# Optimization experiments

Measured on AMD Instinct MI355X. Metric: run time of the kernel, lower is better.

## Reference

```python
import jax, jax.numpy as jnp
import numpy as np

B, C, OUT, H, W, M1, M2, HID = 4, 64, 64, 256, 256, 32, 32, 64
COORD = C + 1  # MLP input: channels + 1 coordinate


def _lin(key, fan_in, fan_out):
    lim = 1.0 / np.sqrt(fan_in)
    kw, kb = jax.random.split(key)
    Wm = jax.random.uniform(kw, (fan_in, fan_out), minval=-lim, maxval=lim, dtype=jnp.float32)
    b = jax.random.uniform(kb, (fan_out,), minval=-lim, maxval=lim, dtype=jnp.float32)
    return Wm, b


def setup_inputs() -> dict:
    key = jax.random.key(0)
    ks = jax.random.split(key, 12)
    x = jax.random.normal(ks[0], (B, C, H, W), dtype=jnp.float32)
    # basis_w MLP: (C+1) -> HID -> HID -> 2*M2
    wW0, wb0 = _lin(ks[1], COORD, HID)
    wW1, wb1 = _lin(ks[2], HID, HID)
    wW2, wb2 = _lin(ks[3], HID, 2 * M2)
    # basis_h MLP: (C+1) -> HID -> HID -> 2*M1
    hW0, hb0 = _lin(ks[4], COORD, HID)
    hW1, hb1 = _lin(ks[5], HID, HID)
    hW2, hb2 = _lin(ks[6], HID, 2 * M1)
    std = (1.0 / (C + OUT)) ** 0.5
    Wf_re = std * jax.random.normal(ks[7], (C, OUT, M1, M2), dtype=jnp.float32)
    Wf_im = std * jax.random.normal(ks[8], (C, OUT, M1, M2), dtype=jnp.float32)
    mixer_w, mixer_b = _lin(ks[9], OUT, OUT)
    mixer_w = mixer_w.T  # (out, in) conv1x1 layout
    sc_w, sc_b = _lin(ks[10], C, OUT)
    sc_w = sc_w.T
    return {
        "x": x,
        "wW0": wW0, "wb0": wb0, "wW1": wW1, "wb1": wb1, "wW2": wW2, "wb2": wb2,
        "hW0": hW0, "hb0": hb0, "hW1": hW1, "hb1": hb1, "hW2": hW2, "hb2": hb2,
        "Wf_re": Wf_re, "Wf_im": Wf_im,
        "mixer_w": mixer_w, "mixer_b": mixer_b,
        "sc_w": sc_w, "sc_b": sc_b,
    }


def _gelu(v):
    return jax.nn.gelu(v, approximate=False)  # torch GELU is exact erf


def _cmlp(x, W0, b0, W1, b1, W2, b2, m):
    h = _gelu(x @ W0 + b0)
    h = _gelu(h @ W1 + b1)
    o = h @ W2 + b2
    return jax.lax.complex(o[..., :m], o[..., m:])


def reference(x, wW0, wb0, wW1, wb1, wW2, wb2,
              hW0, hb0, hW1, hb1, hW2, hb2,
              Wf_re, Wf_im, mixer_w, mixer_b, sc_w, sc_b):
    Bb, Cc, Hh, Ww = x.shape
    # --- W-direction basis: input is (values, w-coord) per pixel ---
    wc = jnp.linspace(-1.0, 1.0, Ww, dtype=jnp.float32)
    w_in = jnp.concatenate(
        [jnp.transpose(x, (0, 2, 3, 1)),
         jnp.broadcast_to(wc[None, None, :, None], (Bb, Hh, Ww, 1))], axis=-1)
    wb = _cmlp(w_in, wW0, wb0, wW1, wb1, wW2, wb2, M2)  # (B,H,W,m2) complex
    xc = x.astype(jnp.complex64)
    # separable transform along W: contract W against runtime basis
    tfw = jnp.einsum('bchw,bhwm->bchm', xc, wb)  # (B,C,H,m2)
    # --- H-direction basis: input is real part of W-transform + h-coord ---
    hcv = jnp.linspace(-1.0, 1.0, Hh, dtype=jnp.float32)
    h_in = jnp.concatenate(
        [jnp.transpose(tfw.real, (0, 3, 2, 1)),
         jnp.broadcast_to(hcv[None, None, :, None], (Bb, M2, Hh, 1))], axis=-1)
    hb = _cmlp(h_in, hW0, hb0, hW1, hb1, hW2, hb2, M1)  # (B,m2,H,m1) complex
    tfhw = jnp.einsum('bchm,bmhk->bckm', tfw, hb)  # (B,C,m1,m2)
    Wf = jax.lax.complex(Wf_re, Wf_im)  # (C_in, C_out, m1, m2)
    proc = jnp.einsum('bixy,oixy->boxy', tfhw, Wf)  # (B,out,m1,m2)
    # inverse transforms with conjugate-transposed bases
    rec = jnp.einsum('bokm,bmhk->bohm', proc, jnp.conj(hb))  # (B,out,H,m2)
    spatial = jnp.einsum('bohm,bhwm->bohw', rec, jnp.conj(wb)).real / (Hh * Ww)
    y = jnp.einsum('bchw,oc->bohw', spatial, mixer_w) + mixer_b[None, :, None, None]
    y = _gelu(y)
    y = y + jnp.einsum('bchw,oc->bohw', x, sc_w) + sc_b[None, :, None, None]
    return _gelu(y)
```

## Files before the change

### kernel.cpp

```cpp
#include <hip/hip_runtime.h>
#include <math.h>


typedef __attribute__((ext_vector_type(8))) short bf16x8;
typedef __attribute__((ext_vector_type(4))) float f32x4;

__device__ __forceinline__ float gelu_f(float v) {
    const float u = v * 0.70710678118654752440f;
    const float xa = fabsf(u);
    const float t = __builtin_amdgcn_rcpf(fmaf(0.3275911f, xa, 1.0f));
    float p = fmaf(1.061405429f, t, -1.453152027f);
    p = fmaf(p, t, 1.421413741f);
    p = fmaf(p, t, -0.284496736f);
    p = fmaf(p, t, 0.254829592f);
    p *= t;
    const float e = __expf(-xa * xa);
    float erfv = fmaf(-p, e, 1.0f);
    erfv = (u < 0.0f) ? -erfv : erfv;
    return 0.5f * v * (1.0f + erfv);
}

__device__ __forceinline__ unsigned short f2b(float f) {
    union { float f; unsigned int u; } v; v.f = f;
    unsigned int u = v.u + 0x7FFFu + ((v.u >> 16) & 1u);
    return (unsigned short)(u >> 16);
}
__device__ __forceinline__ float b2f(unsigned short b) {
    union { unsigned int u; float f; } v; v.u = ((unsigned int)b) << 16;
    return v.f;
}

__device__ __forceinline__ void stage_xT(const float* __restrict__ x,
    unsigned short* __restrict__ sA, int b, int h, int w0, int t, int LD)
{
    const int lane = t & 63, wv = t >> 6;
    const int g = lane >> 4, wg = lane & 15;
#pragma unroll
    for (int r = 0; r < 4; ++r) {
        const int cb = r * 16 + wv * 4;
        const float4 v = *(const float4*)&x[((size_t)(b * 64 + cb + g) * 256 + h) * 256 + w0 + wg * 4];
        const float bx = __shfl_xor(v.x, 16);
        const float by = __shfl_xor(v.y, 16);
        const float bz = __shfl_xor(v.z, 16);
        const float bw = __shfl_xor(v.w, 16);
        float4 s1;
        s1.x = ((g & 1) == 0) ? v.x : by;
        s1.y = ((g & 1) == 0) ? bx  : v.y;
        s1.z = ((g & 1) == 0) ? v.z : bw;
        s1.w = ((g & 1) == 0) ? bz  : v.w;
        const float cx = __shfl_xor(s1.x, 32);
        const float cy = __shfl_xor(s1.y, 32);
        const float cz = __shfl_xor(s1.z, 32);
        const float cw = __shfl_xor(s1.w, 32);
        float4 s2;
        s2.x = ((g & 2) == 0) ? s1.x : cz;
        s2.y = ((g & 2) == 0) ? s1.y : cw;
        s2.z = ((g & 2) == 0) ? cx   : s1.z;
        s2.w = ((g & 2) == 0) ? cy   : s1.w;
        ushort4 u;
        u.x = f2b(s2.x); u.y = f2b(s2.y); u.z = f2b(s2.z); u.w = f2b(s2.w);
        *(ushort4*)&sA[(wg * 4 + g) * LD + cb] = u;
    }
}

__global__ void k_prep(const float* __restrict__ wW0, const float* __restrict__ wW1,
                       const float* __restrict__ wW2,
                       const float* __restrict__ hW0, const float* __restrict__ hW1,
                       const float* __restrict__ hW2,
                       unsigned short* __restrict__ wT0, unsigned short* __restrict__ wT1,
                       unsigned short* __restrict__ wT2,
                       unsigned short* __restrict__ hT0, unsigned short* __restrict__ hT1,
                       unsigned short* __restrict__ hT2)
{
    const int t = threadIdx.x;
    for (int idx = t; idx < 64 * 96; idx += 256) {
        const int o = idx / 96, k = idx % 96;
        wT0[idx] = (k < 65) ? f2b(wW0[k * 64 + o]) : (unsigned short)0;
        hT0[idx] = (k < 65) ? f2b(hW0[k * 64 + o]) : (unsigned short)0;
    }
    for (int idx = t; idx < 4096; idx += 256) {
        const int o = idx >> 6, k = idx & 63;
        wT1[idx] = f2b(wW1[k * 64 + o]);
        wT2[idx] = f2b(wW2[k * 64 + o]);
        hT1[idx] = f2b(hW1[k * 64 + o]);
        hT2[idx] = f2b(hW2[k * 64 + o]);
    }
}

__global__ __launch_bounds__(256) void k_psum(const float* __restrict__ src,
                                              float* __restrict__ dst,
                                              int nparts, int part_stride)
{
    const int i = (blockIdx.x * 256 + threadIdx.x) * 4;
    float4 acc = *(const float4*)&src[i];
    for (int p = 1; p < nparts; ++p) {
        const float4 v = *(const float4*)&src[(size_t)p * part_stride + i];
        acc.x += v.x; acc.y += v.y; acc.z += v.z; acc.w += v.w;
    }
    *(float4*)&dst[i] = acc;
}

__global__ __launch_bounds__(256) void k_psum_procT(const float* __restrict__ src,
                                                    float* __restrict__ dst)
{
    const int idx = blockIdx.x * 256 + threadIdx.x;
    const int o = idx & 63, k = (idx >> 6) & 31, m = (idx >> 11) & 31, b = idx >> 16;
    const size_t in = (size_t)(b * 64 + o) * 1024 + k * 32 + m;
    const float re = src[in] + src[524288 + in];
    const float im = src[262144 + in] + src[524288 + 262144 + in];
    dst[idx] = re;
    dst[262144 + idx] = im;
}

constexpr int MLD = 104;

template<bool GELU, int NKC>
__device__ __forceinline__ void mfma_layer(
    const unsigned short* __restrict__ sW,
    const unsigned short* __restrict__ sAct,
    unsigned short* __restrict__ dst,
    const float* __restrict__ bias, int lane, int wv)
{
    const int arow = lane & 15;
    const int koff = (lane >> 4) * 8;
    const int crow = 16 * wv + (lane >> 4) * 4;
    const f32x4 zero = {0.f, 0.f, 0.f, 0.f};
    f32x4 acc[4] = {zero, zero, zero, zero};
#pragma unroll
    for (int kc = 0; kc < NKC; ++kc) {
        const bf16x8 a = *(const bf16x8*)&sW[(16 * wv + arow) * MLD + kc * 32 + koff];
#pragma unroll
        for (int nt = 0; nt < 4; ++nt) {
            const bf16x8 b = *(const bf16x8*)&sAct[(nt * 16 + arow) * MLD + kc * 32 + koff];
            acc[nt] = __builtin_amdgcn_mfma_f32_16x16x32_bf16(a, b, acc[nt], 0, 0, 0);
        }
    }
    const float4 bv = *(const float4*)&bias[crow];
#pragma unroll
    for (int nt = 0; nt < 4; ++nt) {
        const int px = nt * 16 + arow;
        float v0 = acc[nt][0] + bv.x;
        float v1 = acc[nt][1] + bv.y;
        float v2 = acc[nt][2] + bv.z;
        float v3 = acc[nt][3] + bv.w;
        if (GELU) { v0 = gelu_f(v0); v1 = gelu_f(v1); v2 = gelu_f(v2); v3 = gelu_f(v3); }
        ushort4 u;
        u.x = f2b(v0); u.y = f2b(v1); u.z = f2b(v2); u.w = f2b(v3);
        *(ushort4*)&dst[px * MLD + crow] = u;
    }
}

__device__ __forceinline__ void stage_wT96(const unsigned short* __restrict__ src,
                                           unsigned short* __restrict__ sW, int t) {
#pragma unroll
    for (int r = 0; r < 3; ++r) {
        const int idx = r * 256 + t;
        const int row = idx / 12, f = idx % 12;
        *(uint4*)&sW[row * MLD + f * 8] = *(const uint4*)&src[row * 96 + f * 8];
    }
}
__device__ __forceinline__ void stage_wT64(const unsigned short* __restrict__ src,
                                           unsigned short* __restrict__ sW, int t) {
#pragma unroll
    for (int r = 0; r < 2; ++r) {
        const int idx = r * 256 + t;
        const int row = idx >> 3, f = idx & 7;
        *(uint4*)&sW[row * MLD + f * 8] = *(const uint4*)&src[row * 64 + f * 8];
    }
}

__global__ __launch_bounds__(256) void k_wb_mlp2(
    const float* __restrict__ x,
    const unsigned short* __restrict__ wT0, const float* __restrict__ b0,
    const unsigned short* __restrict__ wT1, const float* __restrict__ b1,
    const unsigned short* __restrict__ wT2, const float* __restrict__ b2,
    unsigned short* __restrict__ wb_bf, unsigned short* __restrict__ wbT)
{
    __shared__ __align__(16) unsigned short sA[64 * MLD];
    __shared__ __align__(16) unsigned short sB[64 * MLD];
    __shared__ __align__(16) unsigned short sW[64 * MLD];
    const int blk = blockIdx.x;
    const int b = blk >> 10, h = (blk >> 2) & 255, wq = blk & 3;
    const int w0 = wq * 64;
    const int t = threadIdx.x;
    const int lane = t & 63, wv = t >> 6;

    stage_xT(x, sA, b, h, w0, t, MLD);
    if (t < 64) {
        const uint4 z = {0, 0, 0, 0};
        *(uint4*)&sA[t * MLD + 64] = z;
        *(uint4*)&sA[t * MLD + 72] = z;
        *(uint4*)&sA[t * MLD + 80] = z;
        *(uint4*)&sA[t * MLD + 88] = z;
        sA[t * MLD + 64] = f2b((float)(w0 + t) * (2.0f / 255.0f) - 1.0f);
    }
    stage_wT96(wT0, sW, t);
    __syncthreads();
    mfma_layer<true, 3>(sW, sA, sB, b0, lane, wv);
    __syncthreads();
    stage_wT64(wT1, sW, t);
    __syncthreads();
    mfma_layer<true, 2>(sW, sB, sA, b1, lane, wv);
    __syncthreads();
    stage_wT64(wT2, sW, t);
    __syncthreads();
    {
        const int arow = lane & 15;
        const int koff = (lane >> 4) * 8;
        const int crow = 16 * wv + (lane >> 4) * 4;
        const f32x4 zero = {0.f, 0.f, 0.f, 0.f};
        f32x4 acc[4] = {zero, zero, zero, zero};
#pragma unroll
        for (int kc = 0; kc < 2; ++kc) {
            const bf16x8 a = *(const bf16x8*)&sW[(16 * wv + arow) * MLD + kc * 32 + koff];
#pragma unroll
            for (int nt = 0; nt < 4; ++nt) {
                const bf16x8 bb = *(const bf16x8*)&sA[(nt * 16 + arow) * MLD + kc * 32 + koff];
                acc[nt] = __builtin_amdgcn_mfma_f32_16x16x32_bf16(a, bb, acc[nt], 0, 0, 0);
            }
        }
        const float4 bv = *(const float4*)&b2[crow];
        const size_t tb2 = (size_t)(b * 256 + h) * 16384;
#pragma unroll
        for (int nt = 0; nt < 4; ++nt) {
            const int px = nt * 16 + arow;
            ushort4 u;
            u.x = f2b(acc[nt][0] + bv.x);
            u.y = f2b(acc[nt][1] + bv.y);
            u.z = f2b(acc[nt][2] + bv.z);
            u.w = f2b(acc[nt][3] + bv.w);
            *(ushort4*)&sB[px * MLD + crow] = u;
            wbT[tb2 + (size_t)(crow + 0) * 256 + w0 + px] = u.x;
            wbT[tb2 + (size_t)(crow + 1) * 256 + w0 + px] = u.y;
            wbT[tb2 + (size_t)(crow + 2) * 256 + w0 + px] = u.z;
            wbT[tb2 + (size_t)(crow + 3) * 256 + w0 + px] = u.w;
        }
    }
    __syncthreads();

    const size_t pixbase = (size_t)(b * 256 + h) * 256 + w0;
#pragma unroll
    for (int r = 0; r < 2; ++r) {
        const int idx = r * 256 + t;
        const int px = idx >> 3, f = idx & 7;
        *(uint4*)&wb_bf[(pixbase + px) * 64 + f * 8] = *(const uint4*)&sB[px * MLD + f * 8];
    }
}

__global__ __launch_bounds__(256) void k_tfw2(
    const float* __restrict__ x,
    const unsigned short* __restrict__ wbT,
    float* __restrict__ tfwM)
{
    constexpr int TLD = 264;
    __shared__ __align__(16) unsigned short sW[64 * TLD];
    __shared__ __align__(16) unsigned short sX[64 * TLD];
    const int bh = blockIdx.x;
    const int b = bh >> 8, h = bh & 255;
    const int t = threadIdx.x;
    const int lane = t & 63, wv = t >> 6;

    const size_t wtb = (size_t)bh * 16384;
#pragma unroll
    for (int r = 0; r < 8; ++r) {
        const int idx = r * 256 + t;
        const int row = idx >> 5, f = idx & 31;
        *(uint4*)&sW[row * TLD + f * 8] = *(const uint4*)&wbT[wtb + (size_t)row * 256 + f * 8];
    }
#pragma unroll
    for (int r = 0; r < 16; ++r) {
        const int idx = r * 256 + t;
        const int c = idx >> 6, f = idx & 63;
        const float4 v = *(const float4*)&x[((size_t)(b * 64 + c) * 256 + h) * 256 + f * 4];
        ushort4 u; u.x = f2b(v.x); u.y = f2b(v.y); u.z = f2b(v.z); u.w = f2b(v.w);
        *(ushort4*)&sX[c * TLD + f * 4] = u;
    }
    __syncthreads();

    const int arow = lane & 15;
    const int koff = (lane >> 4) * 8;
    const f32x4 zero = {0.f, 0.f, 0.f, 0.f};
    f32x4 acc[4] = {zero, zero, zero, zero};
#pragma unroll
    for (int kc = 0; kc < 8; ++kc) {
        const bf16x8 a = *(const bf16x8*)&sW[(16 * wv + arow) * TLD + kc * 32 + koff];
#pragma unroll
        for (int nt = 0; nt < 4; ++nt) {
            const bf16x8 bb = *(const bf16x8*)&sX[(nt * 16 + arow) * TLD + kc * 32 + koff];
            acc[nt] = __builtin_amdgcn_mfma_f32_16x16x32_bf16(a, bb, acc[nt], 0, 0, 0);
        }
    }
    __syncthreads();
    float* sF = (float*)sW;
    const int crow = 16 * wv + (lane >> 4) * 4;
#pragma unroll
    for (int nt = 0; nt < 4; ++nt) {
        const int c = nt * 16 + arow;
#pragma unroll
        for (int j = 0; j < 4; ++j)
            sF[(crow + j) * 68 + c] = acc[nt][j];
    }
    __syncthreads();
#pragma unroll
    for (int r = 0; r < 4; ++r) {
        const int idx = r * 256 + t;
        const int m = idx >> 5, g = idx & 31;
        float4 v;
        v.x = sF[m * 68 + g * 2];
        v.y = sF[(m + 32) * 68 + g * 2];
        v.z = sF[m * 68 + g * 2 + 1];
        v.w = sF[(m + 32) * 68 + g * 2 + 1];
        *(float4*)&tfwM[((size_t)(b * 32 + m) * 256 + h) * 128 + g * 4] = v;
    }
}

__global__ __launch_bounds__(256) void k_hb_mlp2(
    const float* __restrict__ tfwM,
    const unsigned short* __restrict__ hT0, const float* __restrict__ b0,
    const unsigned short* __restrict__ hT1, const float* __restrict__ b1,
    const unsigned short* __restrict__ hT2, const float* __restrict__ b2,
    unsigned short* __restrict__ hb_bf)
{
    __shared__ __align__(16) unsigned short sA[64 * MLD];
    __shared__ __align__(16) unsigned short sB[64 * MLD];
    __shared__ __align__(16) unsigned short sW[64 * MLD];
    const int blk = blockIdx.x;
    const int bm = blk >> 2, hq = blk & 3;
    const int h0 = hq * 64;
    const int t = threadIdx.x;
    const int lane = t & 63, wv = t >> 6;

#pragma unroll
    for (int r = 0; r < 4; ++r) {
        const int idx = r * 256 + t;
        const int p = idx >> 4, f = idx & 15;
        const float* src = &tfwM[(size_t)(bm * 256 + h0 + p) * 128 + f * 8];
        const float4 u0 = *(const float4*)&src[0];
        const float4 u1 = *(const float4*)&src[4];
        ushort4 u;
        u.x = f2b(u0.x); u.y = f2b(u0.z); u.z = f2b(u1.x); u.w = f2b(u1.z);
        *(ushort4*)&sA[p * MLD + f * 4] = u;
    }
    if (t < 64) {
        const uint4 z = {0, 0, 0, 0};
        *(uint4*)&sA[t * MLD + 64] = z;
        *(uint4*)&sA[t * MLD + 72] = z;
        *(uint4*)&sA[t * MLD + 80] = z;
        *(uint4*)&sA[t * MLD + 88] = z;
        sA[t * MLD + 64] = f2b((float)(h0 + t) * (2.0f / 255.0f) - 1.0f);
    }
    stage_wT96(hT0, sW, t);
    __syncthreads();
    mfma_layer<true, 3>(sW, sA, sB, b0, lane, wv);
    __syncthreads();
    stage_wT64(hT1, sW, t);
    __syncthreads();
    mfma_layer<true, 2>(sW, sB, sA, b1, lane, wv);
    __syncthreads();
    stage_wT64(hT2, sW, t);
    __syncthreads();
    mfma_layer<false, 2>(sW, sA, sB, b2, lane, wv);
    __syncthreads();

    const size_t pixbase = (size_t)bm * 256 + h0;
#pragma unroll
    for (int r = 0; r < 2; ++r) {
        const int idx = r * 256 + t;
        const int px = idx >> 3, f = idx & 7;
        *(uint4*)&hb_bf[(pixbase + px) * 64 + f * 8] = *(const uint4*)&sB[px * MLD + f * 8];
    }
}

__global__ __launch_bounds__(256) void k_tfhw3(
    const float* __restrict__ tfwM,
    const unsigned short* __restrict__ hb_bf,
    float* __restrict__ tfhw_p)
{
    __shared__ float hr[64 * 32];
    __shared__ float hi2[64 * 32];
    __shared__ float slab[32 * 64];
    const int blk = blockIdx.x;
    const int bm = blk >> 3, chalf = (blk >> 2) & 1, hq = blk & 3;
    const int b = bm >> 5, m = bm & 31;
    const int t = threadIdx.x;
#pragma unroll
    for (int r = 0; r < 2; ++r) {
        const int q = r * 256 + t;
        const int hl = q >> 3, f = q & 7;
        const uint4 raw = *(const uint4*)&hb_bf[((size_t)bm * 256 + hq * 64 + hl) * 64 + f * 8];
        const unsigned short* us = (const unsigned short*)&raw;
        float v[8];
#pragma unroll
        for (int j = 0; j < 8; ++j) v[j] = b2f(us[j]);
        float* dst = (f < 4) ? &hr[hl * 32 + f * 8] : &hi2[hl * 32 + (f - 4) * 8];
        float4 lo; lo.x = v[0]; lo.y = v[1]; lo.z = v[2]; lo.w = v[3];
        float4 hi; hi.x = v[4]; hi.y = v[5]; hi.z = v[6]; hi.w = v[7];
        *(float4*)&dst[0] = lo;
        *(float4*)&dst[4] = hi;
    }
    const int k = t & 31, cq = t >> 5;
    float accr[4] = {0.f, 0.f, 0.f, 0.f}, acci[4] = {0.f, 0.f, 0.f, 0.f};
    const size_t tbase = (size_t)bm * 32768;
    for (int ht = 0; ht < 2; ++ht) {
        __syncthreads();
#pragma unroll
        for (int r = 0; r < 2; ++r) {
            const int q = r * 256 + t;
            const int hl = q >> 3, f = q & 7;
            *(float4*)&slab[hl * 64 + f * 4] =
                *(const float4*)&tfwM[tbase + (size_t)(hq * 64 + ht * 32 + hl) * 128 + chalf * 64 + f * 4];
        }
        __syncthreads();
#pragma unroll 8
        for (int hl = 0; hl < 32; ++hl) {
            const float hrv = hr[(ht * 32 + hl) * 32 + k];
            const float hiv = hi2[(ht * 32 + hl) * 32 + k];
            const float4 u0 = *(const float4*)&slab[hl * 64 + cq * 8];
            const float4 u1 = *(const float4*)&slab[hl * 64 + cq * 8 + 4];
            accr[0] = fmaf(u0.x, hrv, fmaf(-u0.y, hiv, accr[0]));
            acci[0] = fmaf(u0.x, hiv, fmaf( u0.y, hrv, acci[0]));
            accr[1] = fmaf(u0.z, hrv, fmaf(-u0.w, hiv, accr[1]));
            acci[1] = fmaf(u0.z, hiv, fmaf( u0.w, hrv, acci[1]));
            accr[2] = fmaf(u1.x, hrv, fmaf(-u1.y, hiv, accr[2]));
            acci[2] = fmaf(u1.x, hiv, fmaf( u1.y, hrv, acci[2]));
            accr[3] = fmaf(u1.z, hrv, fmaf(-u1.w, hiv, accr[3]));
            acci[3] = fmaf(u1.z, hiv, fmaf( u1.w, hrv, acci[3]));
        }
    }
    float* tp = tfhw_p + (size_t)hq * 524288;
#pragma unroll
    for (int i = 0; i < 4; ++i) {
        const int c = chalf * 32 + cq * 4 + i;
        const size_t po = ((size_t)(b * 64 + c) * 32 + k) * 32 + m;
        tp[po] = accr[i];
        tp[262144 + po] = acci[i];
    }
}

__global__ __launch_bounds__(256) void k_proc2(
    const float* __restrict__ tfhw,
    const float* __restrict__ Wf_re, const float* __restrict__ Wf_im,
    float* __restrict__ proc_p)
{
    const int blk = blockIdx.x;
    const int o = blk >> 3, kq = (blk >> 1) & 3, chalf = blk & 1;
    const int t = threadIdx.x;
    const int mo = kq * 256 + t;
    const float* tre = tfhw;
    const float* tim = tfhw + 262144;
    float accr[4] = {0.f, 0.f, 0.f, 0.f}, acci[4] = {0.f, 0.f, 0.f, 0.f};
    for (int cc = 0; cc < 32; ++cc) {
        const int c = chalf * 32 + cc;
        const float wfr = Wf_re[(size_t)(c * 64 + o) * 1024 + mo];
        const float wfi = Wf_im[(size_t)(c * 64 + o) * 1024 + mo];
#pragma unroll
        for (int bb = 0; bb < 4; ++bb) {
            const float tr = tre[(size_t)(bb * 64 + c) * 1024 + mo];
            const float ti = tim[(size_t)(bb * 64 + c) * 1024 + mo];
            accr[bb] = fmaf(tr, wfr, fmaf(-ti, wfi, accr[bb]));
            acci[bb] = fmaf(tr, wfi, fmaf(ti, wfr, acci[bb]));
        }
    }
    float* pp = proc_p + (size_t)chalf * 524288;
#pragma unroll
    for (int bb = 0; bb < 4; ++bb) {
        pp[(size_t)(bb * 64 + o) * 1024 + mo] = accr[bb];
        pp[262144 + (size_t)(bb * 64 + o) * 1024 + mo] = acci[bb];
    }
}

__global__ __launch_bounds__(256) void k_rec4(
    const float* __restrict__ procT,
    const unsigned short* __restrict__ hb_bf,
    unsigned short* __restrict__ recO)
{
    __shared__ float lhr[32 * 32];
    __shared__ float lhi[32 * 32];
    const int blk = blockIdx.x;
    const int bm = blk >> 3, hq = blk & 7;
    const int b = bm >> 5, m = bm & 31;
    const int t = threadIdx.x;
    {
        const int hl = t >> 3, f = t & 7;
        const uint4 raw = *(const uint4*)&hb_bf[((size_t)bm * 256 + hq * 32 + hl) * 64 + f * 8];
        const unsigned short* us = (const unsigned short*)&raw;
        float v[8];
#pragma unroll
        for (int j = 0; j < 8; ++j) v[j] = b2f(us[j]);
        float* dst = (f < 4) ? &lhr[hl * 32 + f * 8] : &lhi[hl * 32 + (f - 4) * 8];
        float4 lo; lo.x = v[0]; lo.y = v[1]; lo.z = v[2]; lo.w = v[3];
        float4 hi; hi.x = v[4]; hi.y = v[5]; hi.z = v[6]; hi.w = v[7];
        *(float4*)&dst[0] = lo;
        *(float4*)&dst[4] = hi;
    }
    const int o = t & 63, hg = t >> 6;
    const float* pr = procT + (size_t)(b * 32 + m) * 2048 + o;
    const float* pi = pr + 262144;
    float Pr[32], Pi[32];
#pragma unroll
    for (int k = 0; k < 32; ++k) {
        Pr[k] = pr[k * 64];
        Pi[k] = pi[k * 64];
    }
    __syncthreads();
    for (int hh = 0; hh < 8; ++hh) {
        const int hl = hg * 8 + hh;
        float ar = 0.f, ai = 0.f;
#pragma unroll
        for (int k4 = 0; k4 < 8; ++k4) {
            const float4 hr4 = *(const float4*)&lhr[hl * 32 + k4 * 4];
            const float4 hi4 = *(const float4*)&lhi[hl * 32 + k4 * 4];
            ar = fmaf(Pr[k4*4+0], hr4.x, fmaf(Pi[k4*4+0], hi4.x, ar));
            ai = fmaf(Pi[k4*4+0], hr4.x, fmaf(-Pr[k4*4+0], hi4.x, ai));
            ar = fmaf(Pr[k4*4+1], hr4.y, fmaf(Pi[k4*4+1], hi4.y, ar));
            ai = fmaf(Pi[k4*4+1], hr4.y, fmaf(-Pr[k4*4+1], hi4.y, ai));
            ar = fmaf(Pr[k4*4+2], hr4.z, fmaf(Pi[k4*4+2], hi4.z, ar));
            ai = fmaf(Pi[k4*4+2], hr4.z, fmaf(-Pr[k4*4+2], hi4.z, ai));
            ar = fmaf(Pr[k4*4+3], hr4.w, fmaf(Pi[k4*4+3], hi4.w, ar));
            ai = fmaf(Pi[k4*4+3], hr4.w, fmaf(-Pr[k4*4+3], hi4.w, ai));
        }
        const int h = hq * 32 + hl;
        const size_t rb = ((size_t)(b * 256 + h) * 64 + o) * 64;
        recO[rb + m]      = f2b(ar);
        recO[rb + 32 + m] = f2b(ai);
    }
}

__global__ __launch_bounds__(256) void k_final4(
    const float* __restrict__ x,
    const unsigned short* __restrict__ wb_bf,
    const unsigned short* __restrict__ recO,
    const float* __restrict__ mw, const float* __restrict__ mb,
    const float* __restrict__ scw, const float* __restrict__ scb,
    float* __restrict__ out)
{
    constexpr int LD = 72;
    __shared__ __align__(16) unsigned short sWb[64 * LD];
    __shared__ __align__(16) unsigned short sR [64 * LD];
    __shared__ __align__(16) unsigned short sX [64 * LD];
    __shared__ __align__(16) unsigned short sS [64 * LD];
    const int blk = blockIdx.x;
    const int b = blk >> 10, h = (blk >> 2) & 255, wq = blk & 3;
    const int w0 = wq * 64;
    const int t = threadIdx.x;
    const int lane = t & 63, wv = t >> 6;
    const size_t pixbase = (size_t)(b * 256 + h) * 256 + w0;

#pragma unroll
    for (int r = 0; r < 2; ++r) {
        const int idx = r * 256 + t;
        const int px = idx >> 3, f = idx & 7;
        *(uint4*)&sWb[px * LD + f * 8] = *(const uint4*)&wb_bf[(pixbase + px) * 64 + f * 8];
    }
    const size_t recbase = (size_t)(b * 256 + h) * 4096;
#pragma unroll
    for (int r = 0; r < 2; ++r) {
        const int idx = r * 256 + t;
        const int o = idx >> 3, f = idx & 7;
        *(uint4*)&sR[o * LD + f * 8] = *(const uint4*)&recO[recbase + (size_t)o * 64 + f * 8];
    }
    stage_xT(x, sX, b, h, w0, t, LD);
    __syncthreads();

    const int arow = lane & 15;
    const int koff = (lane >> 4) * 8;
    const f32x4 zero = {0.f, 0.f, 0.f, 0.f};

    f32x4 accA[4] = {zero, zero, zero, zero};
#pragma unroll
    for (int kc = 0; kc < 2; ++kc) {
        const bf16x8 a = *(const bf16x8*)&sR[(16 * wv + arow) * LD + kc * 32 + koff];
#pragma unroll
        for (int nt = 0; nt < 4; ++nt) {
            const bf16x8 bb = *(const bf16x8*)&sWb[(nt * 16 + arow) * LD + kc * 32 + koff];
            accA[nt] = __builtin_amdgcn_mfma_f32_16x16x32_bf16(a, bb, accA[nt], 0, 0, 0);
        }
    }
    __syncthreads();

    const int crow = 16 * wv + (lane >> 4) * 4;
#pragma unroll
    for (int nt = 0; nt < 4; ++nt) {
        const int px = nt * 16 + arow;
#pragma unroll
        for (int j = 0; j < 4; ++j)
            sS[px * LD + crow + j] = f2b(accA[nt][j] * (1.0f / 65536.0f));
    }
#pragma unroll
    for (int r = 0; r < 4; ++r) {
        const int idx = r * 256 + t;
        const int o = idx >> 4, cq = idx & 15;
        const float4 v1 = *(const float4*)&mw[o * 64 + cq * 4];
        ushort4 u1;
        u1.x = f2b(v1.x); u1.y = f2b(v1.y); u1.z = f2b(v1.z); u1.w = f2b(v1.w);
        *(ushort4*)&sWb[o * LD + cq * 4] = u1;
        const float4 v2 = *(const float4*)&scw[o * 64 + cq * 4];
        ushort4 u2;
        u2.x = f2b(v2.x); u2.y = f2b(v2.y); u2.z = f2b(v2.z); u2.w = f2b(v2.w);
        *(ushort4*)&sR[o * LD + cq * 4] = u2;
    }
    __syncthreads();

    f32x4 accB[4] = {zero, zero, zero, zero};
    f32x4 accC[4] = {zero, zero, zero, zero};
#pragma unroll
    for (int kc = 0; kc < 2; ++kc) {
        const bf16x8 am = *(const bf16x8*)&sWb[(16 * wv + arow) * LD + kc * 32 + koff];
        const bf16x8 as = *(const bf16x8*)&sR [(16 * wv + arow) * LD + kc * 32 + koff];
#pragma unroll
        for (int nt = 0; nt < 4; ++nt) {
            const bf16x8 bs = *(const bf16x8*)&sS[(nt * 16 + arow) * LD + kc * 32 + koff];
            const bf16x8 bx = *(const bf16x8*)&sX[(nt * 16 + arow) * LD + kc * 32 + koff];
            accB[nt] = __builtin_amdgcn_mfma_f32_16x16x32_bf16(am, bs, accB[nt], 0, 0, 0);
            accC[nt] = __builtin_amdgcn_mfma_f32_16x16x32_bf16(as, bx, accC[nt], 0, 0, 0);
        }
    }

#pragma unroll
    for (int nt = 0; nt < 4; ++nt) {
        const int px = nt * 16 + arow;
#pragma unroll
        for (int j = 0; j < 4; ++j) {
            const int o = crow + j;
            const float y = gelu_f(accB[nt][j] + mb[o]);
            const float z = y + accC[nt][j] + scb[o];
            out[((size_t)(b * 64 + o) * 256 + h) * 256 + w0 + px] = gelu_f(z);
        }
    }
}

extern "C" void kernel_launch(void* const* d_in, const int* in_sizes, int n_in,
                              void* d_out, int out_size, void* d_ws, size_t ws_size,
                              hipStream_t stream) {
    const float* x    = (const float*)d_in[0];
    const float* wW0  = (const float*)d_in[1];
    const float* wb0  = (const float*)d_in[2];
    const float* wW1  = (const float*)d_in[3];
    const float* wb1  = (const float*)d_in[4];
    const float* wW2  = (const float*)d_in[5];
    const float* wb2  = (const float*)d_in[6];
    const float* hW0  = (const float*)d_in[7];
    const float* hb0  = (const float*)d_in[8];
    const float* hW1  = (const float*)d_in[9];
    const float* hb1  = (const float*)d_in[10];
    const float* hW2  = (const float*)d_in[11];
    const float* hb2  = (const float*)d_in[12];
    const float* Wf_re = (const float*)d_in[13];
    const float* Wf_im = (const float*)d_in[14];
    const float* mw   = (const float*)d_in[15];
    const float* mbv  = (const float*)d_in[16];
    const float* scw  = (const float*)d_in[17];
    const float* scb  = (const float*)d_in[18];

    char* base = (char*)d_ws;
    unsigned short* wb_bf = (unsigned short*)(base + 0);
    unsigned short* wbT   = (unsigned short*)(base + 33554432);
    float* tfwM   = (float*)(base + 67108864);
    unsigned short* hb_bf = (unsigned short*)(base + 83886080);
    float* tfhw_p = (float*)(base + 88080384);
    float* tfhw   = (float*)(base + 96468992);
    float* proc_p = (float*)(base + 98566144);
    float* procT  = (float*)(base + 102760448);
    unsigned short* recO = (unsigned short*)(base + 104857600);
    unsigned short* wT0 = (unsigned short*)(base + 113246208);
    unsigned short* wT1 = (unsigned short*)(base + 113258496);
    unsigned short* wT2 = (unsigned short*)(base + 113266688);
    unsigned short* hT0 = (unsigned short*)(base + 113274880);
    unsigned short* hT1 = (unsigned short*)(base + 113287168);
    unsigned short* hT2 = (unsigned short*)(base + 113295360);

    k_prep<<<1, 256, 0, stream>>>(wW0, wW1, wW2, hW0, hW1, hW2,
                                  wT0, wT1, wT2, hT0, hT1, hT2);
    k_wb_mlp2<<<4096, 256, 0, stream>>>(x, wT0, wb0, wT1, wb1, wT2, wb2, wb_bf, wbT);
    k_tfw2<<<1024, 256, 0, stream>>>(x, wbT, tfwM);
    k_hb_mlp2<<<512, 256, 0, stream>>>(tfwM, hT0, hb0, hT1, hb1, hT2, hb2, hb_bf);
    k_tfhw3<<<1024, 256, 0, stream>>>(tfwM, hb_bf, tfhw_p);
    k_psum<<<1024, 256, 0, stream>>>(tfhw_p, tfhw, 4, 524288);
    k_proc2<<<512, 256, 0, stream>>>(tfhw, Wf_re, Wf_im, proc_p);
    k_psum_procT<<<1024, 256, 0, stream>>>(proc_p, procT);
    k_rec4<<<1024, 256, 0, stream>>>(procT, hb_bf, recO);
    k_final4<<<4096, 256, 0, stream>>>(x, wb_bf, recO, mw, mbv, scw, scb, (float*)d_out);
}
```

Baseline: 195.5 us.

## Fuse W-basis MLP with W-direction transform to drop transposed basis buffer

```diff
diff --git a/kernel.cpp b/kernel.cpp
--- a/kernel.cpp
+++ b/kernel.cpp
@@ -30,36 +30,44 @@
     return v.f;
 }
 
+constexpr int MLD = 104;
+constexpr int XLD = 72;
+
+__device__ __forceinline__ ushort4 butterfly_xT(const float4 v, int q) {
+    const float bx = __shfl_xor(v.x, 1);
+    const float by = __shfl_xor(v.y, 1);
+    const float bz = __shfl_xor(v.z, 1);
+    const float bw = __shfl_xor(v.w, 1);
+    float4 s1;
+    s1.x = ((q & 1) == 0) ? v.x : by;
+    s1.y = ((q & 1) == 0) ? bx  : v.y;
+    s1.z = ((q & 1) == 0) ? v.z : bw;
+    s1.w = ((q & 1) == 0) ? bz  : v.w;
+    const float cx = __shfl_xor(s1.x, 2);
+    const float cy = __shfl_xor(s1.y, 2);
+    const float cz = __shfl_xor(s1.z, 2);
+    const float cw = __shfl_xor(s1.w, 2);
+    float4 s2;
+    s2.x = ((q & 2) == 0) ? s1.x : cz;
+    s2.y = ((q & 2) == 0) ? s1.y : cw;
+    s2.z = ((q & 2) == 0) ? cx   : s1.z;
+    s2.w = ((q & 2) == 0) ? cy   : s1.w;
+    ushort4 u;
+    u.x = f2b(s2.x); u.y = f2b(s2.y); u.z = f2b(s2.z); u.w = f2b(s2.w);
+    return u;
+}
+
 __device__ __forceinline__ void stage_xT(const float* __restrict__ x,
     unsigned short* __restrict__ sA, int b, int h, int w0, int t, int LD)
 {
     const int lane = t & 63, wv = t >> 6;
-    const int g = lane >> 4, wg = lane & 15;
+    const int q = lane & 3, wg = lane >> 2;
 #pragma unroll
     for (int r = 0; r < 4; ++r) {
-        const int cb = r * 16 + wv * 4;
-        const float4 v = *(const float4*)&x[((size_t)(b * 64 + cb + g) * 256 + h) * 256 + w0 + wg * 4];
-        const float bx = __shfl_xor(v.x, 16);
-        const float by = __shfl_xor(v.y, 16);
-        const float bz = __shfl_xor(v.z, 16);
-        const float bw = __shfl_xor(v.w, 16);
-        float4 s1;
-        s1.x = ((g & 1) == 0) ? v.x : by;
-        s1.y = ((g & 1) == 0) ? bx  : v.y;
-        s1.z = ((g & 1) == 0) ? v.z : bw;
-        s1.w = ((g & 1) == 0) ? bz  : v.w;
-        const float cx = __shfl_xor(s1.x, 32);
-        const float cy = __shfl_xor(s1.y, 32);
-        const float cz = __shfl_xor(s1.z, 32);
-        const float cw = __shfl_xor(s1.w, 32);
-        float4 s2;
-        s2.x = ((g & 2) == 0) ? s1.x : cz;
-        s2.y = ((g & 2) == 0) ? s1.y : cw;
-        s2.z = ((g & 2) == 0) ? cx   : s1.z;
-        s2.w = ((g & 2) == 0) ? cy   : s1.w;
-        ushort4 u;
-        u.x = f2b(s2.x); u.y = f2b(s2.y); u.z = f2b(s2.z); u.w = f2b(s2.w);
-        *(ushort4*)&sA[(wg * 4 + g) * LD + cb] = u;
+        const int cb = (r * 4 + wv) * 4;
+        const float4 v = *(const float4*)&x[((size_t)(b * 64 + cb + q) * 256 + h) * 256 + w0 + wg * 4];
+        const ushort4 u = butterfly_xT(v, q);
+        *(ushort4*)&sA[(wg * 4 + q) * LD + cb] = u;
     }
 }
 
@@ -111,8 +119,6 @@
     dst[idx] = re;
     dst[262144 + idx] = im;
 }
-
-constexpr int MLD = 104;
 
 template<bool GELU, int NKC>
 __device__ __forceinline__ void mfma_layer(
@@ -169,136 +175,120 @@
     }
 }
 
-__global__ __launch_bounds__(256) void k_wb_mlp2(
+__global__ __launch_bounds__(256) void k_wbtfw(
     const float* __restrict__ x,
     const unsigned short* __restrict__ wT0, const float* __restrict__ b0,
     const unsigned short* __restrict__ wT1, const float* __restrict__ b1,
     const unsigned short* __restrict__ wT2, const float* __restrict__ b2,
-    unsigned short* __restrict__ wb_bf, unsigned short* __restrict__ wbT)
-{
-    __shared__ __align__(16) unsigned short sA[64 * MLD];
-    __shared__ __align__(16) unsigned short sB[64 * MLD];
-    __shared__ __align__(16) unsigned short sW[64 * MLD];
-    const int blk = blockIdx.x;
-    const int b = blk >> 10, h = (blk >> 2) & 255, wq = blk & 3;
-    const int w0 = wq * 64;
-    const int t = threadIdx.x;
-    const int lane = t & 63, wv = t >> 6;
-
-    stage_xT(x, sA, b, h, w0, t, MLD);
-    if (t < 64) {
-        const uint4 z = {0, 0, 0, 0};
-        *(uint4*)&sA[t * MLD + 64] = z;
-        *(uint4*)&sA[t * MLD + 72] = z;
-        *(uint4*)&sA[t * MLD + 80] = z;
-        *(uint4*)&sA[t * MLD + 88] = z;
-        sA[t * MLD + 64] = f2b((float)(w0 + t) * (2.0f / 255.0f) - 1.0f);
-    }
-    stage_wT96(wT0, sW, t);
-    __syncthreads();
-    mfma_layer<true, 3>(sW, sA, sB, b0, lane, wv);
-    __syncthreads();
-    stage_wT64(wT1, sW, t);
-    __syncthreads();
-    mfma_layer<true, 2>(sW, sB, sA, b1, lane, wv);
-    __syncthreads();
-    stage_wT64(wT2, sW, t);
-    __syncthreads();
-    {
-        const int arow = lane & 15;
-        const int koff = (lane >> 4) * 8;
-        const int crow = 16 * wv + (lane >> 4) * 4;
-        const f32x4 zero = {0.f, 0.f, 0.f, 0.f};
-        f32x4 acc[4] = {zero, zero, zero, zero};
-#pragma unroll
-        for (int kc = 0; kc < 2; ++kc) {
-            const bf16x8 a = *(const bf16x8*)&sW[(16 * wv + arow) * MLD + kc * 32 + koff];
-#pragma unroll
-            for (int nt = 0; nt < 4; ++nt) {
-                const bf16x8 bb = *(const bf16x8*)&sA[(nt * 16 + arow) * MLD + kc * 32 + koff];
-                acc[nt] = __builtin_amdgcn_mfma_f32_16x16x32_bf16(a, bb, acc[nt], 0, 0, 0);
-            }
-        }
-        const float4 bv = *(const float4*)&b2[crow];
-        const size_t tb2 = (size_t)(b * 256 + h) * 16384;
-#pragma unroll
-        for (int nt = 0; nt < 4; ++nt) {
-            const int px = nt * 16 + arow;
-            ushort4 u;
-            u.x = f2b(acc[nt][0] + bv.x);
-            u.y = f2b(acc[nt][1] + bv.y);
-            u.z = f2b(acc[nt][2] + bv.z);
-            u.w = f2b(acc[nt][3] + bv.w);
-            *(ushort4*)&sB[px * MLD + crow] = u;
-            wbT[tb2 + (size_t)(crow + 0) * 256 + w0 + px] = u.x;
-            wbT[tb2 + (size_t)(crow + 1) * 256 + w0 + px] = u.y;
-            wbT[tb2 + (size_t)(crow + 2) * 256 + w0 + px] = u.z;
-            wbT[tb2 + (size_t)(crow + 3) * 256 + w0 + px] = u.w;
-        }
-    }
-    __syncthreads();
-
-    const size_t pixbase = (size_t)(b * 256 + h) * 256 + w0;
-#pragma unroll
-    for (int r = 0; r < 2; ++r) {
-        const int idx = r * 256 + t;
-        const int px = idx >> 3, f = idx & 7;
-        *(uint4*)&wb_bf[(pixbase + px) * 64 + f * 8] = *(const uint4*)&sB[px * MLD + f * 8];
-    }
-}
-
-__global__ __launch_bounds__(256) void k_tfw2(
-    const float* __restrict__ x,
-    const unsigned short* __restrict__ wbT,
-    float* __restrict__ tfwM)
-{
-    constexpr int TLD = 264;
-    __shared__ __align__(16) unsigned short sW[64 * TLD];
-    __shared__ __align__(16) unsigned short sX[64 * TLD];
+    unsigned short* __restrict__ wb_bf, float* __restrict__ tfwM)
+{
+    __shared__ __align__(16) unsigned short smem[6656 * 3 + 4608 * 2];
+    unsigned short* sA   = smem;
+    unsigned short* sB   = smem + 6656;
+    unsigned short* sW   = smem + 13312;
+    unsigned short* sXt  = smem + 19968;
+    unsigned short* sWBt = smem + 24576;
+
     const int bh = blockIdx.x;
     const int b = bh >> 8, h = bh & 255;
     const int t = threadIdx.x;
     const int lane = t & 63, wv = t >> 6;
-
-    const size_t wtb = (size_t)bh * 16384;
-#pragma unroll
-    for (int r = 0; r < 8; ++r) {
-        const int idx = r * 256 + t;
-        const int row = idx >> 5, f = idx & 31;
-        *(uint4*)&sW[row * TLD + f * 8] = *(const uint4*)&wbT[wtb + (size_t)row * 256 + f * 8];
-    }
-#pragma unroll
-    for (int r = 0; r < 16; ++r) {
-        const int idx = r * 256 + t;
-        const int c = idx >> 6, f = idx & 63;
-        const float4 v = *(const float4*)&x[((size_t)(b * 64 + c) * 256 + h) * 256 + f * 4];
-        ushort4 u; u.x = f2b(v.x); u.y = f2b(v.y); u.z = f2b(v.z); u.w = f2b(v.w);
-        *(ushort4*)&sX[c * TLD + f * 4] = u;
-    }
-    __syncthreads();
-
     const int arow = lane & 15;
     const int koff = (lane >> 4) * 8;
+    const int crow = 16 * wv + (lane >> 4) * 4;
     const f32x4 zero = {0.f, 0.f, 0.f, 0.f};
-    f32x4 acc[4] = {zero, zero, zero, zero};
-#pragma unroll
-    for (int kc = 0; kc < 8; ++kc) {
-        const bf16x8 a = *(const bf16x8*)&sW[(16 * wv + arow) * TLD + kc * 32 + koff];
-#pragma unroll
-        for (int nt = 0; nt < 4; ++nt) {
-            const bf16x8 bb = *(const bf16x8*)&sX[(nt * 16 + arow) * TLD + kc * 32 + koff];
-            acc[nt] = __builtin_amdgcn_mfma_f32_16x16x32_bf16(a, bb, acc[nt], 0, 0, 0);
-        }
-    }
-    __syncthreads();
-    float* sF = (float*)sW;
-    const int crow = 16 * wv + (lane >> 4) * 4;
+
+    f32x4 atf[4] = {zero, zero, zero, zero};
+
+    for (int wq = 0; wq < 4; ++wq) {
+        const int w0 = wq * 64;
+        __syncthreads();
+        {
+            const int q = lane & 3, wg = lane >> 2;
+#pragma unroll
+            for (int r = 0; r < 4; ++r) {
+                const int cb = (r * 4 + wv) * 4;
+                const int c = cb + q;
+                const float4 v = *(const float4*)&x[((size_t)(b * 64 + c) * 256 + h) * 256 + w0 + wg * 4];
+                ushort4 ux;
+                ux.x = f2b(v.x); ux.y = f2b(v.y); ux.z = f2b(v.z); ux.w = f2b(v.w);
+                *(ushort4*)&sXt[c * XLD + wg * 4] = ux;
+                const ushort4 u = butterfly_xT(v, q);
+                *(ushort4*)&sA[(wg * 4 + q) * MLD + cb] = u;
+            }
+        }
+        if (t < 64) {
+            const uint4 z = {0, 0, 0, 0};
+            *(uint4*)&sA[t * MLD + 64] = z;
+            *(uint4*)&sA[t * MLD + 72] = z;
+            *(uint4*)&sA[t * MLD + 80] = z;
+            *(uint4*)&sA[t * MLD + 88] = z;
+            sA[t * MLD + 64] = f2b((float)(w0 + t) * (2.0f / 255.0f) - 1.0f);
+        }
+        stage_wT96(wT0, sW, t);
+        __syncthreads();
+        mfma_layer<true, 3>(sW, sA, sB, b0, lane, wv);
+        __syncthreads();
+        stage_wT64(wT1, sW, t);
+        __syncthreads();
+        mfma_layer<true, 2>(sW, sB, sA, b1, lane, wv);
+        __syncthreads();
+        stage_wT64(wT2, sW, t);
+        __syncthreads();
+        {
+            f32x4 acc[4] = {zero, zero, zero, zero};
+#pragma unroll
+            for (int kc = 0; kc < 2; ++kc) {
+                const bf16x8 a = *(const bf16x8*)&sW[(16 * wv + arow) * MLD + kc * 32 + koff];
+#pragma unroll
+                for (int nt = 0; nt < 4; ++nt) {
+                    const bf16x8 bb = *(const bf16x8*)&sA[(nt * 16 + arow) * MLD + kc * 32 + koff];
+                    acc[nt] = __builtin_amdgcn_mfma_f32_16x16x32_bf16(a, bb, acc[nt], 0, 0, 0);
+                }
+            }
+            const float4 bv = *(const float4*)&b2[crow];
+#pragma unroll
+            for (int nt = 0; nt < 4; ++nt) {
+                const int px = nt * 16 + arow;
+                ushort4 u;
+                u.x = f2b(acc[nt][0] + bv.x);
+                u.y = f2b(acc[nt][1] + bv.y);
+                u.z = f2b(acc[nt][2] + bv.z);
+                u.w = f2b(acc[nt][3] + bv.w);
+                *(ushort4*)&sB[px * MLD + crow] = u;
+                sWBt[(crow + 0) * XLD + px] = u.x;
+                sWBt[(crow + 1) * XLD + px] = u.y;
+                sWBt[(crow + 2) * XLD + px] = u.z;
+                sWBt[(crow + 3) * XLD + px] = u.w;
+            }
+        }
+        __syncthreads();
+        const size_t pixbase = (size_t)(b * 256 + h) * 256 + w0;
+#pragma unroll
+        for (int r = 0; r < 2; ++r) {
+            const int idx = r * 256 + t;
+            const int px = idx >> 3, f = idx & 7;
+            *(uint4*)&wb_bf[(pixbase + px) * 64 + f * 8] = *(const uint4*)&sB[px * MLD + f * 8];
+        }
+#pragma unroll
+        for (int kc = 0; kc < 2; ++kc) {
+            const bf16x8 a = *(const bf16x8*)&sWBt[(16 * wv + arow) * XLD + kc * 32 + koff];
+#pragma unroll
+            for (int nt = 0; nt < 4; ++nt) {
+                const bf16x8 bb = *(const bf16x8*)&sXt[(nt * 16 + arow) * XLD + kc * 32 + koff];
+                atf[nt] = __builtin_amdgcn_mfma_f32_16x16x32_bf16(a, bb, atf[nt], 0, 0, 0);
+            }
+        }
+    }
+
+    __syncthreads();
+    float* sF = (float*)smem;
 #pragma unroll
     for (int nt = 0; nt < 4; ++nt) {
         const int c = nt * 16 + arow;
 #pragma unroll
         for (int j = 0; j < 4; ++j)
-            sF[(crow + j) * 68 + c] = acc[nt][j];
+            sF[(crow + j) * 68 + c] = atf[nt][j];
     }
     __syncthreads();
 #pragma unroll
@@ -323,7 +313,7 @@
 {
     __shared__ __align__(16) unsigned short sA[64 * MLD];
     __shared__ __align__(16) unsigned short sB[64 * MLD];
-    __shared__ __align__(16) unsigned short sW[64 * MLD];
+    __shared__ __align__(16) unsigned short sW[65 * MLD];
     const int blk = blockIdx.x;
     const int bm = blk >> 2, hq = blk & 3;
     const int h0 = hq * 64;
@@ -654,25 +644,23 @@
 
     char* base = (char*)d_ws;
     unsigned short* wb_bf = (unsigned short*)(base + 0);
-    unsigned short* wbT   = (unsigned short*)(base + 33554432);
-    float* tfwM   = (float*)(base + 67108864);
-    unsigned short* hb_bf = (unsigned short*)(base + 83886080);
-    float* tfhw_p = (float*)(base + 88080384);
-    float* tfhw   = (float*)(base + 96468992);
-    float* proc_p = (float*)(base + 98566144);
-    float* procT  = (float*)(base + 102760448);
-    unsigned short* recO = (unsigned short*)(base + 104857600);
-    unsigned short* wT0 = (unsigned short*)(base + 113246208);
-    unsigned short* wT1 = (unsigned short*)(base + 113258496);
-    unsigned short* wT2 = (unsigned short*)(base + 113266688);
-    unsigned short* hT0 = (unsigned short*)(base + 113274880);
-    unsigned short* hT1 = (unsigned short*)(base + 113287168);
-    unsigned short* hT2 = (unsigned short*)(base + 113295360);
+    float* tfwM   = (float*)(base + 33554432);
+    unsigned short* hb_bf = (unsigned short*)(base + 50331648);
+    float* tfhw_p = (float*)(base + 54525952);
+    float* tfhw   = (float*)(base + 62914560);
+    float* proc_p = (float*)(base + 65011712);
+    float* procT  = (float*)(base + 69206016);
+    unsigned short* recO = (unsigned short*)(base + 71303168);
+    unsigned short* wT0 = (unsigned short*)(base + 79691776);
+    unsigned short* wT1 = (unsigned short*)(base + 79704064);
+    unsigned short* wT2 = (unsigned short*)(base + 79712256);
+    unsigned short* hT0 = (unsigned short*)(base + 79720448);
+    unsigned short* hT1 = (unsigned short*)(base + 79732736);
+    unsigned short* hT2 = (unsigned short*)(base + 79740928);
 
     k_prep<<<1, 256, 0, stream>>>(wW0, wW1, wW2, hW0, hW1, hW2,
                                   wT0, wT1, wT2, hT0, hT1, hT2);
-    k_wb_mlp2<<<4096, 256, 0, stream>>>(x, wT0, wb0, wT1, wb1, wT2, wb2, wb_bf, wbT);
-    k_tfw2<<<1024, 256, 0, stream>>>(x, wbT, tfwM);
+    k_wbtfw<<<1024, 256, 0, stream>>>(x, wT0, wb0, wT1, wb1, wT2, wb2, wb_bf, tfwM);
     k_hb_mlp2<<<512, 256, 0, stream>>>(tfwM, hT0, hb0, hT1, hb1, hT2, hb2, hb_bf);
     k_tfhw3<<<1024, 256, 0, stream>>>(tfwM, hb_bf, tfhw_p);
     k_psum<<<1024, 256, 0, stream>>>(tfhw_p, tfhw, 4, 524288);
```

New measurement: 186.5 us. -4.6%, faster.
